# Kernel optimization log

Measured on AMD Instinct MI355X. Metric: run time of the kernel, lower is better.

The kernel has to match this reference:

```python
import jax, jax.numpy as jnp
import numpy as np

N = 2048
T = 4000
MAX_SPIKES = 512
V_RESET = 1.0
ALPHA = 0.01


def setup_inputs() -> dict:
    key = jax.random.key(0)
    k1, k2, k3, k4, k5 = jax.random.split(key, 5)
    ts = jnp.arange(T, dtype=jnp.float32) * (1.0 / T)  # [T] grid over [0, 1)
    v0 = 0.1 * jax.random.normal(k1, (N,), dtype=jnp.float32)
    i0 = 0.1 * jax.random.normal(k2, (N,), dtype=jnp.float32)
    ic = jax.random.uniform(k3, (N,), dtype=jnp.float32, minval=0.5, maxval=1.5)
    # _build_w: uniform weights in [0.5, 1), network mask all-False -> no zeroing
    w = jax.random.uniform(k4, (N, N), dtype=jnp.float32, minval=0.5, maxval=1.0)
    mu = jax.random.uniform(k5, (2,), dtype=jnp.float32, minval=0.5, maxval=1.0)
    return {"ts": ts, "v0": v0, "i0": i0, "ic": ic, "w": w, "mu": mu,
            "seed": 0, "max_spikes": MAX_SPIKES}


def reference(ts, v0, i0, ic, w, mu, seed, max_spikes):
    n = v0.shape[0]
    key = jax.random.key(seed)
    k_init, k_trans = jax.random.split(key)
    # s0 = log(U) - alpha  (negative; spike when s crosses 0)
    s0 = jnp.log(jax.random.uniform(k_init, (n,))) - ALPHA
    y0 = jnp.stack([v0, i0, s0], axis=-1)  # [n, 3]

    dts = ts[1:] - ts[:-1]
    steps = jnp.arange(ts.shape[0] - 1)
    tev0 = jnp.full((max_spikes,), jnp.inf, dtype=ts.dtype)
    yev0 = jnp.full((max_spikes, n, 3), jnp.inf, dtype=y0.dtype)
    et0 = jnp.zeros((max_spikes, n), dtype=bool)

    def drift(y):
        v, i, s = y[:, 0], y[:, 1], y[:, 2]
        dv = mu[0] * (i + ic - v)
        di = -mu[1] * i
        ds = jax.nn.softplus(v)  # intensity_fn
        return jnp.stack([dv, di, ds], axis=-1)

    def step(carry, inp):
        y, nsp, tev, yev, et = carry
        t_next, dt, idx = inp
        y1 = y + dt * drift(y)                 # Euler step
        ev = y1[:, 2] >= 0.0                   # cond_fn: y[n, 2] root crossing
        has = jnp.any(ev)
        eidx = jnp.argmax(ev)
        u = jax.random.uniform(jax.random.fold_in(k_trans, idx), (n,))
        # trans_fn: reset v, add weight row to all i, resample s for spikers
        v_t = y1[:, 0] - jnp.where(ev, V_RESET, 0.0)
        i_t = y1[:, 1] + w[eidx]
        s_t = jnp.where(ev, jnp.log(u) - ALPHA, y1[:, 2])
        y2 = jnp.where(has, jnp.stack([v_t, i_t, s_t], axis=-1), y1)
        rec = has & (nsp < max_spikes)
        widx = jnp.minimum(nsp, max_spikes - 1)
        tev = tev.at[widx].set(jnp.where(rec, t_next, tev[widx]))
        yev = yev.at[widx].set(jnp.where(rec, y1, yev[widx]))
        et = et.at[widx].set(jnp.where(rec, ev, et[widx]))
        nsp = nsp + has.astype(jnp.int32)
        return (y2, nsp, tev, yev, et), y2

    init = (y0, jnp.int32(0), tev0, yev0, et0)
    (_, num_spikes, tevents, yevents, event_types), ys_rest = jax.lax.scan(
        step, init, (ts[1:], dts, steps))
    ys = jnp.concatenate([y0[None], ys_rest], axis=0)  # [T, n, 3]
    return ys, tevents, yevents, event_types, num_spikes
```

## Files before the change

### kernel.cpp

```cpp
#include <hip/hip_runtime.h>
#include <stdint.h>

#define XLA_LOG_TAIL_A 1
#define XLA_USE_FMA    0

#if XLA_USE_FMA
#define MADD(a,b,c) __builtin_fmaf((a),(b),(c))
#else
#define MADD(a,b,c) ((a)*(b)+(c))
#endif

#define N_NEUR 2048
#define HALF_N 1024
#define CKPT   124

__device__ __forceinline__ uint32_t rotl32(uint32_t x, int r) {
  return (x << r) | (x >> (32 - r));
}

__device__ __forceinline__ void tf2x32(uint32_t k0, uint32_t k1,
                                       uint32_t& x0, uint32_t& x1) {
  const uint32_t k2 = k0 ^ k1 ^ 0x1BD11BDAu;
  x0 += k0; x1 += k1;
#define TF_R(r) { x0 += x1; x1 = rotl32(x1, r); x1 ^= x0; }
  TF_R(13) TF_R(15) TF_R(26) TF_R(6)
  x0 += k1; x1 += k2 + 1u;
  TF_R(17) TF_R(29) TF_R(16) TF_R(24)
  x0 += k2; x1 += k0 + 2u;
  TF_R(13) TF_R(15) TF_R(26) TF_R(6)
  x0 += k0; x1 += k1 + 3u;
  TF_R(17) TF_R(29) TF_R(16) TF_R(24)
  x0 += k1; x1 += k2 + 4u;
  TF_R(13) TF_R(15) TF_R(26) TF_R(6)
  x0 += k2; x1 += k0 + 5u;
#undef TF_R
}

__device__ __forceinline__ float u01_from_bits(uint32_t bits) {
#pragma clang fp contract(off)
  float f = __uint_as_float((bits >> 9) | 0x3f800000u);
  return f - 1.0f;
}

__device__ __forceinline__ float xla_log(float xin) {
#pragma clang fp contract(off)
  float t0 = fmaxf(xin, __uint_as_float(0x00800000u));
  uint32_t bits = __float_as_uint(t0);
  int em = (int)(bits >> 23) - 127;
  t0 = __uint_as_float((bits & 0x807fffffu) | 0x3f000000u);
  float e = 1.0f + (float)em;
  const bool mlt = t0 < (float)0.707106781186547524;
  float tmp1 = mlt ? t0 : 0.0f;
  t0 = t0 - 1.0f;
  e = e - (mlt ? 1.0f : 0.0f);
  t0 = t0 + tmp1;
  float x2 = t0 * t0;
  float x3 = x2 * t0;
  float y  = MADD(t0, (float)7.0376836292E-2, (float)-1.1514610310E-1);
  float ya = MADD(t0, (float)-1.2420140846E-1, (float)1.4249322787E-1);
  float yb = MADD(t0, (float)2.0000714765E-1, (float)-2.4999993993E-1);
  y  = MADD(y,  t0, (float)1.1676998740E-1);
  ya = MADD(ya, t0, (float)-1.6668057665E-1);
  yb = MADD(yb, t0, (float)3.3333331174E-1);
  y  = MADD(y, x3, ya);
  y  = MADD(y, x3, yb);
  y  = y * x3;
  float ey1 = e * (float)-2.12194440e-4;
  float hx2 = x2 * 0.5f;
  y = y + ey1;
  t0 = t0 - hx2;
  float ey2 = e * (float)0.693359375;
#if XLA_LOG_TAIL_A
  t0 = t0 + y;
  t0 = t0 + ey2;
#else
  t0 = t0 + ey2;
  t0 = t0 + y;
#endif
  if (xin == 0.0f) return -__builtin_inff();
  return t0;
}

__device__ __forceinline__ float xla_exp(float xin) {
#pragma clang fp contract(off)
  float x = fmaxf(xin, (float)-88.3762626647949);
  x = fminf(x, (float)88.3762626647950);
  float fx = floorf(MADD(x, (float)1.44269504088896341, 0.5f));
  float tmp = (float)0.693359375 * fx;
  float z = (float)-2.12194440e-4 * fx;
  x = x - tmp;
  x = x - z;
  z = x * x;
  float y = MADD(x, (float)1.9875691500E-4, (float)1.3981999507E-3);
  y = MADD(y, x, (float)8.3334519073E-3);
  y = MADD(y, x, (float)4.1665795894E-2);
  y = MADD(y, x, (float)1.6666665459E-1);
  y = MADD(y, x, (float)5.0000001201E-1);
  y = MADD(y, z, x);
  y = 1.0f + y;
  int n = (int)fx;
  float p2n = __uint_as_float((uint32_t)(n + 127) << 23);
  return fmaxf(y * p2n, xin);
}

__device__ __forceinline__ float xla_log1p(float x) {
#pragma clang fp contract(off)
  float fl = xla_log(x + 1.0f);
  float fs = ((-0.5f * x) + 1.0f) * x;
  return (fabsf(x) < (float)1e-4) ? fs : fl;
}

__device__ __forceinline__ float softplus_xla(float v) {
#pragma clang fp contract(off)
  if (v >= 16.0f) return v;
  float a = fabsf(v);
  float ex = xla_exp(-a);
  float lp = xla_log1p(ex);
  return fmaxf(v, 0.0f) + lp;
}

__global__ void snn_init(float* __restrict__ out, size_t inf_base,
                         size_t inf_cnt, size_t zero_cnt) {
  size_t i = (size_t)blockIdx.x * blockDim.x + threadIdx.x;
  size_t stride = (size_t)gridDim.x * blockDim.x;
  size_t total = inf_cnt + zero_cnt;
  for (size_t k = i; k < total; k += stride) {
    out[inf_base + k] = (k < inf_cnt) ? __builtin_inff() : 0.0f;
  }
}

__global__ __launch_bounds__(1024)
void snn_pre(const int* __restrict__ seedp, float* __restrict__ sres) {
#pragma clang fp contract(off)
  const int step = blockIdx.x;
  const int t = threadIdx.x;
  uint32_t seed = (uint32_t)seedp[0];
  uint32_t a0 = 0u, a1 = 2u; tf2x32(0u, seed, a0, a1);
  uint32_t b0 = 1u, b1 = 3u; tf2x32(0u, seed, b0, b1);
  uint32_t f0 = 0u, f1 = (uint32_t)step; tf2x32(a1, b1, f0, f1);
  uint32_t d0 = (uint32_t)t, d1 = (uint32_t)(t + HALF_N);
  tf2x32(f0, f1, d0, d1);
  float srA = xla_log(u01_from_bits(d0)) - 0.01f;
  float srB = xla_log(u01_from_bits(d1)) - 0.01f;
  sres[(size_t)step * N_NEUR + t] = srA;
  sres[(size_t)step * N_NEUR + HALF_N + t] = srB;
}

__global__ __launch_bounds__(512, 1)
void snn_evt(const float* __restrict__ ts, const float* __restrict__ v0,
             const float* __restrict__ i0, const float* __restrict__ ic,
             const float* __restrict__ w, const float* __restrict__ mu,
             const int* __restrict__ seedp, const float* __restrict__ sres,
             uint32_t* __restrict__ spk, float* __restrict__ out, int T, int MS) {
#pragma clang fp contract(off)
  const int tid = threadIdx.x;
  const int nb = tid * 4;
  const int wave = tid >> 6;
  const int lane = tid & 63;

  float* ys   = out;
  float* tev  = out + (size_t)T * N_NEUR * 3;
  float* etv  = tev + (size_t)MS + (size_t)MS * N_NEUR * 3;
  float* nspp = etv + (size_t)MS * N_NEUR;

  uint32_t seed = (uint32_t)seedp[0];
  uint32_t a0 = 0u, a1 = 2u; tf2x32(0u, seed, a0, a1);
  uint32_t b0 = 1u, b1 = 3u; tf2x32(0u, seed, b0, b1);
  const uint32_t ki0 = a0, ki1 = b0;

  const float m0 = mu[0], m1 = mu[1];

  float vvO[4];
  float ssE[4];
  bool  evO[4];
  float y1iP[4];
  float wEp[4], wOp[4];
  bool  hasEp = false, hasOp = false;
  float dtOp = 0.0f;
  float icv[4];
  float srE[4], srO[4];

  {
    float4 x = *(const float4*)&v0[nb];
    vvO[0]=x.x; vvO[1]=x.y; vvO[2]=x.z; vvO[3]=x.w;
  }
  {
    float4 x = *(const float4*)&i0[nb];
    y1iP[0]=x.x; y1iP[1]=x.y; y1iP[2]=x.z; y1iP[3]=x.w;
  }
  {
    float4 x = *(const float4*)&ic[nb];
    icv[0]=x.x; icv[1]=x.y; icv[2]=x.z; icv[3]=x.w;
  }
#pragma unroll
  for (int q = 0; q < 4; ++q) {
    int j = nb + q;
    uint32_t c0 = (uint32_t)(j < HALF_N ? j : j - HALF_N);
    uint32_t c1 = c0 + HALF_N;
    tf2x32(ki0, ki1, c0, c1);
    ssE[q] = xla_log(u01_from_bits(j < HALF_N ? c0 : c1)) - 0.01f;
    evO[q] = false;
    wEp[q] = 0.0f; wOp[q] = 0.0f;
  }
  {
    float4 x = *(const float4*)(sres + nb);
    srE[0]=x.x; srE[1]=x.y; srE[2]=x.z; srE[3]=x.w;
  }
  {
    float4 x = *(const float4*)(sres + N_NEUR + nb);
    srO[0]=x.x; srO[1]=x.y; srO[2]=x.z; srO[3]=x.w;
  }

  __shared__ alignas(16) uint32_t slot[2][16];
  __syncthreads();

  int nsp = 0;
  int next_ck = 0;
  float tsE = ts[0];
  const int pairs = (T - 1) >> 1;
  const int last_row = T - 2;

  for (int P = 0; P < pairs; ++P) {
    const int e = 2 * P;

    float vvE[4], iiE[4], y1iO_[4];
#pragma unroll
    for (int q = 0; q < 4; ++q) {
      float iiO = hasEp ? (y1iP[q] + wEp[q]) : y1iP[q];
      float dv  = m0 * ((iiO + icv[q]) - vvO[q]);
      float y1v = vvO[q] + dtOp * dv;
      float y1i = iiO + dtOp * ((-m1) * iiO);
      vvE[q] = y1v - (evO[q] ? 1.0f : 0.0f);
      y1iO_[q] = y1i;
    }
#pragma unroll
    for (int q = 0; q < 4; ++q)
      iiE[q] = hasOp ? (y1iO_[q] + wOp[q]) : y1iO_[q];

    if (e == next_ck) {
      float* yr = ys + ((size_t)e * N_NEUR + nb) * 3;
      ((float4*)yr)[0] = make_float4(vvE[0], iiE[0], ssE[0], vvE[1]);
      ((float4*)yr)[1] = make_float4(iiE[1], ssE[1], vvE[2], iiE[2]);
      ((float4*)yr)[2] = make_float4(ssE[2], vvE[3], iiE[3], ssE[3]);
      next_ck += CKPT;
    }

    const float tsE1 = ts[e + 1];
    const float tsE2 = ts[e + 2];
    const float dtE = tsE1 - tsE;
    const float dtO = tsE2 - tsE1;

    float y1iE[4], vvOn[4], ssEn[4];
    bool evE[4], evOn[4];
#pragma unroll
    for (int q = 0; q < 4; ++q) {
      float sp  = softplus_xla(vvE[q]);
      float y1s = ssE[q] + dtE * sp;
      evE[q] = (y1s >= 0.0f);
      float dv  = m0 * ((iiE[q] + icv[q]) - vvE[q]);
      float y1v = vvE[q] + dtE * dv;
      y1iE[q] = iiE[q] + dtE * ((-m1) * iiE[q]);
      vvOn[q] = y1v - (evE[q] ? 1.0f : 0.0f);
      float ssO_ = evE[q] ? srE[q] : y1s;
      float spO = softplus_xla(vvOn[q]);
      float y1sO = ssO_ + dtO * spO;
      evOn[q] = (y1sO >= 0.0f);
      ssEn[q] = evOn[q] ? srO[q] : y1sO;
    }

    {
      int lE = 4;
      if (evE[3]) lE = 3;
      if (evE[2]) lE = 2;
      if (evE[1]) lE = 1;
      if (evE[0]) lE = 0;
      int lO = 4;
      if (evOn[3]) lO = 3;
      if (evOn[2]) lO = 2;
      if (evOn[1]) lO = 1;
      if (evOn[0]) lO = 0;
      unsigned long long bE = __ballot(lE < 4);
      unsigned long long bO = __ballot(lO < 4);
      if (lane == 0) {
        uint32_t cE = 0xFFFFFFFFu, cO = 0xFFFFFFFFu;
        if (bE) cE = (uint32_t)__builtin_amdgcn_readlane(nb + lE, __builtin_ctzll(bE));
        if (bO) cO = (uint32_t)__builtin_amdgcn_readlane(nb + lO, __builtin_ctzll(bO));
        *(uint64_t*)&slot[P & 1][wave * 2] = ((uint64_t)cO << 32) | (uint64_t)cE;
      }
    }
    float srEn[4], srOn[4];
    {
      int re = e + 2;  if (re > last_row) re = last_row;
      int ro = e + 3;  if (ro > last_row) ro = last_row;
      float4 x = *(const float4*)(sres + (size_t)re * N_NEUR + nb);
      srEn[0]=x.x; srEn[1]=x.y; srEn[2]=x.z; srEn[3]=x.w;
      float4 y = *(const float4*)(sres + (size_t)ro * N_NEUR + nb);
      srOn[0]=y.x; srOn[1]=y.y; srOn[2]=y.z; srOn[3]=y.w;
    }

    __syncthreads();

    uint32_t gE, gO;
    {
      const uint4* rp = (const uint4*)&slot[P & 1][0];
      uint4 r0 = rp[0], r1 = rp[1], r2 = rp[2], r3 = rp[3];
      uint32_t a = r0.x < r1.x ? r0.x : r1.x;
      uint32_t b = r2.x < r3.x ? r2.x : r3.x;
      uint32_t c = r0.z < r1.z ? r0.z : r1.z;
      uint32_t d = r2.z < r3.z ? r2.z : r3.z;
      a = a < b ? a : b;  c = c < d ? c : d;
      gE = a < c ? a : c;
      uint32_t e1 = r0.y < r1.y ? r0.y : r1.y;
      uint32_t f1 = r2.y < r3.y ? r2.y : r3.y;
      uint32_t g1 = r0.w < r1.w ? r0.w : r1.w;
      uint32_t h1 = r2.w < r3.w ? r2.w : r3.w;
      e1 = e1 < f1 ? e1 : f1;  g1 = g1 < h1 ? g1 : h1;
      gO = e1 < g1 ? e1 : g1;
    }
    gE = (uint32_t)__builtin_amdgcn_readfirstlane((int)gE);
    gO = (uint32_t)__builtin_amdgcn_readfirstlane((int)gO);
    const bool hasE = (gE != 0xFFFFFFFFu);
    const bool hasO = (gO != 0xFFFFFFFFu);

    if (tid == 0) {
      spk[e] = ((uint32_t)nsp << 16) | (hasE ? (gE & 0xFFFFu) : 0xFFFFu);
      if (hasE && nsp < MS) tev[nsp] = tsE1;
    }
    int nspE = nsp + (hasE ? 1 : 0);
    if (tid == 0) {
      spk[e + 1] = ((uint32_t)nspE << 16) | (hasO ? (gO & 0xFFFFu) : 0xFFFFu);
      if (hasO && nspE < MS) tev[nspE] = tsE2;
    }
    nsp = nspE + (hasO ? 1 : 0);

    float wEn[4] = {0,0,0,0}, wOn[4] = {0,0,0,0};
    if (hasE) {
      float4 x = *(const float4*)&w[((size_t)gE << 11) + nb];
      wEn[0]=x.x; wEn[1]=x.y; wEn[2]=x.z; wEn[3]=x.w;
    }
    if (hasO) {
      float4 x = *(const float4*)&w[((size_t)gO << 11) + nb];
      wOn[0]=x.x; wOn[1]=x.y; wOn[2]=x.z; wOn[3]=x.w;
    }

#pragma unroll
    for (int q = 0; q < 4; ++q) {
      vvO[q] = vvOn[q];
      ssE[q] = ssEn[q];
      evO[q] = evOn[q];
      y1iP[q] = y1iE[q];
      wEp[q] = wEn[q];
      wOp[q] = wOn[q];
      srE[q] = srEn[q];
      srO[q] = srOn[q];
    }
    hasEp = hasE; hasOp = hasO;
    dtOp = dtO;
    tsE = tsE2;
  }

  if ((T - 1) & 1) {
    const int e = T - 2;
    float vvE[4], iiE[4];
#pragma unroll
    for (int q = 0; q < 4; ++q) {
      float iiO = hasEp ? (y1iP[q] + wEp[q]) : y1iP[q];
      float dv  = m0 * ((iiO + icv[q]) - vvO[q]);
      float y1v = vvO[q] + dtOp * dv;
      float y1i = iiO + dtOp * ((-m1) * iiO);
      vvE[q] = y1v - (evO[q] ? 1.0f : 0.0f);
      iiE[q] = hasOp ? (y1i + wOp[q]) : y1i;
    }
    if (e == next_ck) {
      float* yr = ys + ((size_t)e * N_NEUR + nb) * 3;
      ((float4*)yr)[0] = make_float4(vvE[0], iiE[0], ssE[0], vvE[1]);
      ((float4*)yr)[1] = make_float4(iiE[1], ssE[1], vvE[2], iiE[2]);
      ((float4*)yr)[2] = make_float4(ssE[2], vvE[3], iiE[3], ssE[3]);
    }
    const float tsE1 = ts[T - 1];
    const float dtE = tsE1 - tsE;
    bool evE[4];
#pragma unroll
    for (int q = 0; q < 4; ++q) {
      float sp  = softplus_xla(vvE[q]);
      float y1s = ssE[q] + dtE * sp;
      evE[q] = (y1s >= 0.0f);
    }
    int lE = 4;
    if (evE[3]) lE = 3;
    if (evE[2]) lE = 2;
    if (evE[1]) lE = 1;
    if (evE[0]) lE = 0;
    unsigned long long bE = __ballot(lE < 4);
    if (lane == 0) {
      uint32_t cE = 0xFFFFFFFFu;
      if (bE) cE = (uint32_t)__builtin_amdgcn_readlane(nb + lE, __builtin_ctzll(bE));
      *(uint64_t*)&slot[pairs & 1][wave * 2] =
          ((uint64_t)0xFFFFFFFFu << 32) | (uint64_t)cE;
    }
    __syncthreads();
    uint32_t gE;
    {
      const uint4* rp = (const uint4*)&slot[pairs & 1][0];
      uint4 r0 = rp[0], r1 = rp[1], r2 = rp[2], r3 = rp[3];
      uint32_t a = r0.x < r1.x ? r0.x : r1.x;
      uint32_t b = r2.x < r3.x ? r2.x : r3.x;
      uint32_t c = r0.z < r1.z ? r0.z : r1.z;
      uint32_t d = r2.z < r3.z ? r2.z : r3.z;
      a = a < b ? a : b;  c = c < d ? c : d;
      gE = a < c ? a : c;
    }
    gE = (uint32_t)__builtin_amdgcn_readfirstlane((int)gE);
    const bool hasE = (gE != 0xFFFFFFFFu);
    if (tid == 0) {
      spk[e] = ((uint32_t)nsp << 16) | (hasE ? (gE & 0xFFFFu) : 0xFFFFu);
      if (hasE && nsp < MS) tev[nsp] = tsE1;
    }
    nsp += hasE ? 1 : 0;
  }

  if (tid == 0) nspp[0] = (float)nsp;
}

__global__ __launch_bounds__(1024, 1)
void snn_rep(const float* __restrict__ ts, const float* __restrict__ ic,
             const float* __restrict__ w, const float* __restrict__ mu,
             const float* __restrict__ sres, const uint32_t* __restrict__ spk,
             float* __restrict__ out, int T, int MS) {
#pragma clang fp contract(off)
  const int seg = blockIdx.x >> 1;
  const int gn = (blockIdx.x & 1) * 1024 + threadIdx.x;
  const int lo = seg * CKPT;
  const int end = min(lo + CKPT, T - 1);

  float* ys  = out;
  float* tev = out + (size_t)T * N_NEUR * 3;
  float* yev = tev + (size_t)MS;
  float* etv = yev + (size_t)MS * N_NEUR * 3;

  const float* y0r = ys + ((size_t)lo * N_NEUR + gn) * 3;
  float vv = y0r[0];
  float ii = y0r[1];
  float ss = y0r[2];
  const float icv = ic[gn];
  const float m0 = mu[0], m1 = mu[1];
  float tp = ts[lo];

  for (int k = lo; k < end; ++k) {
    const float tn = ts[k + 1];
    const float dt = tn - tp;
    tp = tn;
    const uint32_t pk = spk[k];

    float sp  = softplus_xla(vv);
    float y1s = ss + dt * sp;
    const bool ev = (y1s >= 0.0f);
    float dv  = m0 * ((ii + icv) - vv);
    float y1v = vv + dt * dv;
    float y1i = ii + dt * ((-m1) * ii);

    const uint32_t e16 = pk & 0xFFFFu;
    const bool has = (e16 != 0xFFFFu);
    const uint32_t nsp = pk >> 16;

    float wv = 0.0f;
    if (has) wv = w[((size_t)e16 << 11) + gn];

    if (has && nsp < (uint32_t)MS) {
      float* ye = yev + ((size_t)nsp * N_NEUR + gn) * 3;
      ye[0] = y1v; ye[1] = y1i; ye[2] = y1s;
      etv[(size_t)nsp * N_NEUR + gn] = ev ? 1.0f : 0.0f;
    }

    ii = has ? (y1i + wv) : y1i;
    vv = y1v - (ev ? 1.0f : 0.0f);
    if (ev) ss = sres[(size_t)k * N_NEUR + gn]; else ss = y1s;

    float* yr = ys + ((size_t)(k + 1) * N_NEUR + gn) * 3;
    yr[0] = vv; yr[1] = ii; yr[2] = ss;
  }
}

template <bool USE_SRES>
__global__ __launch_bounds__(1024, 1)
void snn_sim(const float* __restrict__ ts, const float* __restrict__ v0,
             const float* __restrict__ i0, const float* __restrict__ ic,
             const float* __restrict__ w, const float* __restrict__ mu,
             const int* __restrict__ seedp, const float* __restrict__ sres,
             float* __restrict__ out, int T, int MS) {
#pragma clang fp contract(off)
  const int tid = threadIdx.x;
  const int nb = tid * 2;
  const int lane = tid & 63;

  float* ys   = out;
  float* tev  = out + (size_t)T * N_NEUR * 3;
  float* yev  = tev + (size_t)MS;
  float* etv  = yev + (size_t)MS * N_NEUR * 3;
  float* nspp = etv + (size_t)MS * N_NEUR;

  uint32_t seed = (uint32_t)seedp[0];
  uint32_t a0 = 0u, a1 = 2u; tf2x32(0u, seed, a0, a1);
  uint32_t b0 = 1u, b1 = 3u; tf2x32(0u, seed, b0, b1);
  const uint32_t ki0 = a0, ki1 = b0;
  const uint32_t kt0 = a1, kt1 = b1;

  float vv0, vv1, ii0, ii1, ss0, ss1, icv0, icv1;
  { float2 x = *(const float2*)&v0[nb]; vv0 = x.x; vv1 = x.y; }
  { float2 x = *(const float2*)&i0[nb]; ii0 = x.x; ii1 = x.y; }
  { float2 x = *(const float2*)&ic[nb]; icv0 = x.x; icv1 = x.y; }
  {
    uint32_t c0 = (uint32_t)(nb < HALF_N ? nb : nb - HALF_N);
    uint32_t c1 = c0 + HALF_N;
    tf2x32(ki0, ki1, c0, c1);
    ss0 = xla_log(u01_from_bits(nb < HALF_N ? c0 : c1)) - 0.01f;
  }
  {
    int j = nb + 1;
    uint32_t c0 = (uint32_t)(j < HALF_N ? j : j - HALF_N);
    uint32_t c1 = c0 + HALF_N;
    tf2x32(ki0, ki1, c0, c1);
    ss1 = xla_log(u01_from_bits(j < HALF_N ? c0 : c1)) - 0.01f;
  }
  const float m0 = mu[0], m1 = mu[1];

  {
    float* yr = ys + (size_t)nb * 3;
    ((float2*)yr)[0] = make_float2(vv0, ii0);
    ((float2*)yr)[1] = make_float2(ss0, vv1);
    ((float2*)yr)[2] = make_float2(ii1, ss1);
  }

  __shared__ uint32_t slot[4];
  if (tid < 4) slot[tid] = 0xFFFFFFFFu;
  __syncthreads();

  int nsp = 0;
  float tp = ts[0];
  const float* srp = USE_SRES ? (sres + nb) : nullptr;
  float* yrow = ys + (size_t)N_NEUR * 3 + (size_t)nb * 3;

  for (int k = 0; k < T - 1; ++k) {
    const float tn = ts[k + 1];
    const float dt = tn - tp;
    tp = tn;

    float sr0 = 0.0f, sr1 = 0.0f;
    if (USE_SRES) {
      float2 x = *(const float2*)srp;
      sr0 = x.x; sr1 = x.y;
      srp += N_NEUR;
    }

    float sp0 = softplus_xla(vv0);
    float sp1 = softplus_xla(vv1);
    float y1s0 = ss0 + dt * sp0;
    float y1s1 = ss1 + dt * sp1;
    const bool ev0 = (y1s0 >= 0.0f);
    const bool ev1 = (y1s1 >= 0.0f);

    int lidx = ev0 ? 0 : (ev1 ? 1 : 2);
    unsigned long long bm = __ballot(lidx < 2);
    if (lane == 0 && bm) {
      int fl = __builtin_ctzll(bm);
      uint32_t cand = (uint32_t)__builtin_amdgcn_readlane(nb + lidx, fl);
      atomicMin(&slot[k & 3], cand);
    }
    if (tid == 0) slot[(k + 1) & 3] = 0xFFFFFFFFu;

    float dv0 = m0 * ((ii0 + icv0) - vv0);
    float dv1 = m0 * ((ii1 + icv1) - vv1);
    float y1v0 = vv0 + dt * dv0;
    float y1v1 = vv1 + dt * dv1;
    float y1i0 = ii0 + dt * ((-m1) * ii0);
    float y1i1 = ii1 + dt * ((-m1) * ii1);

    __syncthreads();

    uint32_t gmin = (uint32_t)__builtin_amdgcn_readfirstlane((int)slot[k & 3]);
    const bool has = (gmin != 0xFFFFFFFFu);

    float wv0 = 0.0f, wv1 = 0.0f;
    if (has) {
      float2 x = *(const float2*)&w[((size_t)gmin << 11) + nb];
      wv0 = x.x; wv1 = x.y;
    }

    if (has && nsp < MS) {
      if (tid == 0) tev[nsp] = tn;
      float* ye = yev + ((size_t)nsp * N_NEUR + nb) * 3;
      ((float2*)ye)[0] = make_float2(y1v0, y1i0);
      ((float2*)ye)[1] = make_float2(y1s0, y1v1);
      ((float2*)ye)[2] = make_float2(y1i1, y1s1);
      *(float2*)(etv + (size_t)nsp * N_NEUR + nb) =
          make_float2(ev0 ? 1.0f : 0.0f, ev1 ? 1.0f : 0.0f);
    }
    nsp += has ? 1 : 0;

    ii0 = has ? (y1i0 + wv0) : y1i0;
    ii1 = has ? (y1i1 + wv1) : y1i1;
    vv0 = y1v0 - (ev0 ? 1.0f : 0.0f);
    vv1 = y1v1 - (ev1 ? 1.0f : 0.0f);
    if (USE_SRES) {
      ss0 = ev0 ? sr0 : y1s0;
      ss1 = ev1 ? sr1 : y1s1;
    } else {
      ss0 = y1s0; ss1 = y1s1;
      if (ev0 | ev1) {
        uint32_t f0 = 0u, f1 = (uint32_t)k;
        tf2x32(kt0, kt1, f0, f1);
        if (ev0) {
          uint32_t c0 = (uint32_t)(nb < HALF_N ? nb : nb - HALF_N);
          uint32_t c1 = c0 + HALF_N;
          tf2x32(f0, f1, c0, c1);
          ss0 = xla_log(u01_from_bits(nb < HALF_N ? c0 : c1)) - 0.01f;
        }
        if (ev1) {
          int j = nb + 1;
          uint32_t c0 = (uint32_t)(j < HALF_N ? j : j - HALF_N);
          uint32_t c1 = c0 + HALF_N;
          tf2x32(f0, f1, c0, c1);
          ss1 = xla_log(u01_from_bits(j < HALF_N ? c0 : c1)) - 0.01f;
        }
      }
    }

    ((float2*)yrow)[0] = make_float2(vv0, ii0);
    ((float2*)yrow)[1] = make_float2(ss0, vv1);
    ((float2*)yrow)[2] = make_float2(ii1, ss1);
    yrow += (size_t)N_NEUR * 3;
  }

  if (tid == 0) nspp[0] = (float)nsp;
}

extern "C" void kernel_launch(void* const* d_in, const int* in_sizes, int n_in,
                              void* d_out, int out_size, void* d_ws, size_t ws_size,
                              hipStream_t stream) {
  const float* ts = (const float*)d_in[0];
  const float* v0 = (const float*)d_in[1];
  const float* i0 = (const float*)d_in[2];
  const float* ic = (const float*)d_in[3];
  const float* w  = (const float*)d_in[4];
  const float* mu = (const float*)d_in[5];
  const int* seed = (const int*)d_in[6];

  const int T = in_sizes[0];
  const int N = in_sizes[1];
  long long rem = (long long)out_size - (long long)T * N * 3 - 1;
  int MS = (int)(rem / (1 + 4 * (long long)N));
  if (MS <= 0) MS = 512;

  size_t inf_base = (size_t)T * N * 3;
  size_t inf_cnt  = (size_t)MS + (size_t)MS * N * 3;
  size_t zero_cnt = (size_t)MS * N;
  snn_init<<<dim3(512), dim3(256), 0, stream>>>((float*)d_out, inf_base, inf_cnt, zero_cnt);

  size_t sres_bytes = (size_t)(T - 1) * (size_t)N * sizeof(float);
  size_t full_bytes = sres_bytes + (size_t)(T - 1) * sizeof(uint32_t);

  if (ws_size >= full_bytes) {
    float* sres = (float*)d_ws;
    uint32_t* spk = (uint32_t*)((char*)d_ws + sres_bytes);
    snn_pre<<<dim3(T - 1), dim3(1024), 0, stream>>>(seed, sres);
    snn_evt<<<dim3(1), dim3(512), 0, stream>>>(ts, v0, i0, ic, w, mu, seed,
                                               sres, spk, (float*)d_out, T, MS);
    int nseg = (T - 1 + CKPT - 1) / CKPT;
    snn_rep<<<dim3(nseg * 2), dim3(1024), 0, stream>>>(ts, ic, w, mu, sres, spk,
                                                       (float*)d_out, T, MS);
  } else if (ws_size >= sres_bytes) {
    snn_pre<<<dim3(T - 1), dim3(1024), 0, stream>>>(seed, (float*)d_ws);
    snn_sim<true><<<dim3(1), dim3(1024), 0, stream>>>(ts, v0, i0, ic, w, mu, seed,
                                                      (const float*)d_ws,
                                                      (float*)d_out, T, MS);
  } else {
    snn_sim<false><<<dim3(1), dim3(1024), 0, stream>>>(ts, v0, i0, ic, w, mu, seed,
                                                       nullptr, (float*)d_out, T, MS);
  }
}
```

Before: 3.097 ms.

## Widen event kernel to 1024 threads and reduce spike index via LDS atomicMin

The sequential event-detection kernel now runs 1024 threads with two neurons each instead of 512 threads with four, which halves per-thread serial work on the critical path. The per-wave slot array and 16-entry min-reduction after the barrier are replaced by LDS atomicMin into a four-deep ring of slots, each reset two pairs ahead. Loads of the next resample values and timestamps are moved earlier to overlap with compute. In exchange there are more waves per barrier (16 vs 8) and contended atomics on a single LDS word.

```diff
diff --git a/kernel.cpp b/kernel.cpp
--- a/kernel.cpp
+++ b/kernel.cpp
@@ -146,7 +146,7 @@
   sres[(size_t)step * N_NEUR + HALF_N + t] = srB;
 }
 
-__global__ __launch_bounds__(512, 1)
+__global__ __launch_bounds__(1024, 1)
 void snn_evt(const float* __restrict__ ts, const float* __restrict__ v0,
              const float* __restrict__ i0, const float* __restrict__ ic,
              const float* __restrict__ w, const float* __restrict__ mu,
@@ -154,8 +154,7 @@
              uint32_t* __restrict__ spk, float* __restrict__ out, int T, int MS) {
 #pragma clang fp contract(off)
   const int tid = threadIdx.x;
-  const int nb = tid * 4;
-  const int wave = tid >> 6;
+  const int nb = tid * 2;
   const int lane = tid & 63;
 
   float* ys   = out;
@@ -170,30 +169,16 @@
 
   const float m0 = mu[0], m1 = mu[1];
 
-  float vvO[4];
-  float ssE[4];
-  bool  evO[4];
-  float y1iP[4];
-  float wEp[4], wOp[4];
+  float vvO[2], ssE[2], y1iP[2], wEp[2], wOp[2], icv[2], srE[2], srO[2];
+  bool  evO[2];
   bool  hasEp = false, hasOp = false;
   float dtOp = 0.0f;
-  float icv[4];
-  float srE[4], srO[4];
-
-  {
-    float4 x = *(const float4*)&v0[nb];
-    vvO[0]=x.x; vvO[1]=x.y; vvO[2]=x.z; vvO[3]=x.w;
-  }
-  {
-    float4 x = *(const float4*)&i0[nb];
-    y1iP[0]=x.x; y1iP[1]=x.y; y1iP[2]=x.z; y1iP[3]=x.w;
-  }
-  {
-    float4 x = *(const float4*)&ic[nb];
-    icv[0]=x.x; icv[1]=x.y; icv[2]=x.z; icv[3]=x.w;
-  }
+
+  { float2 x = *(const float2*)&v0[nb]; vvO[0]=x.x; vvO[1]=x.y; }
+  { float2 x = *(const float2*)&i0[nb]; y1iP[0]=x.x; y1iP[1]=x.y; }
+  { float2 x = *(const float2*)&ic[nb]; icv[0]=x.x; icv[1]=x.y; }
 #pragma unroll
-  for (int q = 0; q < 4; ++q) {
+  for (int q = 0; q < 2; ++q) {
     int j = nb + q;
     uint32_t c0 = (uint32_t)(j < HALF_N ? j : j - HALF_N);
     uint32_t c1 = c0 + HALF_N;
@@ -202,16 +187,11 @@
     evO[q] = false;
     wEp[q] = 0.0f; wOp[q] = 0.0f;
   }
-  {
-    float4 x = *(const float4*)(sres + nb);
-    srE[0]=x.x; srE[1]=x.y; srE[2]=x.z; srE[3]=x.w;
-  }
-  {
-    float4 x = *(const float4*)(sres + N_NEUR + nb);
-    srO[0]=x.x; srO[1]=x.y; srO[2]=x.z; srO[3]=x.w;
-  }
-
-  __shared__ alignas(16) uint32_t slot[2][16];
+  { float2 x = *(const float2*)(sres + nb);          srE[0]=x.x; srE[1]=x.y; }
+  { float2 x = *(const float2*)(sres + N_NEUR + nb); srO[0]=x.x; srO[1]=x.y; }
+
+  __shared__ alignas(8) uint32_t slot[4][2];
+  if (tid < 8) ((uint32_t*)slot)[tid] = 0xFFFFFFFFu;
   __syncthreads();
 
   int nsp = 0;
@@ -223,9 +203,25 @@
   for (int P = 0; P < pairs; ++P) {
     const int e = 2 * P;
 
-    float vvE[4], iiE[4], y1iO_[4];
+    const float tsE1 = ts[e + 1];
+    const float tsE2 = ts[e + 2];
+    float srEn[2], srOn[2];
+    {
+      int re = e + 2;  if (re > last_row) re = last_row;
+      int ro = e + 3;  if (ro > last_row) ro = last_row;
+      float2 x = *(const float2*)(sres + (size_t)re * N_NEUR + nb);
+      srEn[0]=x.x; srEn[1]=x.y;
+      float2 y = *(const float2*)(sres + (size_t)ro * N_NEUR + nb);
+      srOn[0]=y.x; srOn[1]=y.y;
+    }
+    if (tid == 0) {
+      slot[(P + 2) & 3][0] = 0xFFFFFFFFu;
+      slot[(P + 2) & 3][1] = 0xFFFFFFFFu;
+    }
+
+    float vvE[2], iiE[2], y1iO_[2];
 #pragma unroll
-    for (int q = 0; q < 4; ++q) {
+    for (int q = 0; q < 2; ++q) {
       float iiO = hasEp ? (y1iP[q] + wEp[q]) : y1iP[q];
       float dv  = m0 * ((iiO + icv[q]) - vvO[q]);
       float y1v = vvO[q] + dtOp * dv;
@@ -234,26 +230,24 @@
       y1iO_[q] = y1i;
     }
 #pragma unroll
-    for (int q = 0; q < 4; ++q)
+    for (int q = 0; q < 2; ++q)
       iiE[q] = hasOp ? (y1iO_[q] + wOp[q]) : y1iO_[q];
 
     if (e == next_ck) {
       float* yr = ys + ((size_t)e * N_NEUR + nb) * 3;
-      ((float4*)yr)[0] = make_float4(vvE[0], iiE[0], ssE[0], vvE[1]);
-      ((float4*)yr)[1] = make_float4(iiE[1], ssE[1], vvE[2], iiE[2]);
-      ((float4*)yr)[2] = make_float4(ssE[2], vvE[3], iiE[3], ssE[3]);
+      ((float2*)yr)[0] = make_float2(vvE[0], iiE[0]);
+      ((float2*)yr)[1] = make_float2(ssE[0], vvE[1]);
+      ((float2*)yr)[2] = make_float2(iiE[1], ssE[1]);
       next_ck += CKPT;
     }
 
-    const float tsE1 = ts[e + 1];
-    const float tsE2 = ts[e + 2];
     const float dtE = tsE1 - tsE;
     const float dtO = tsE2 - tsE1;
 
-    float y1iE[4], vvOn[4], ssEn[4];
-    bool evE[4], evOn[4];
+    float y1iE[2], vvOn[2], ssEn[2];
+    bool evE[2], evOn[2];
 #pragma unroll
-    for (int q = 0; q < 4; ++q) {
+    for (int q = 0; q < 2; ++q) {
       float sp  = softplus_xla(vvE[q]);
       float y1s = ssE[q] + dtE * sp;
       evE[q] = (y1s >= 0.0f);
@@ -269,56 +263,27 @@
     }
 
     {
-      int lE = 4;
-      if (evE[3]) lE = 3;
-      if (evE[2]) lE = 2;
-      if (evE[1]) lE = 1;
-      if (evE[0]) lE = 0;
-      int lO = 4;
-      if (evOn[3]) lO = 3;
-      if (evOn[2]) lO = 2;
-      if (evOn[1]) lO = 1;
-      if (evOn[0]) lO = 0;
-      unsigned long long bE = __ballot(lE < 4);
-      unsigned long long bO = __ballot(lO < 4);
+      int lE = evE[0] ? 0 : (evE[1] ? 1 : 2);
+      int lO = evOn[0] ? 0 : (evOn[1] ? 1 : 2);
+      unsigned long long bE = __ballot(lE < 2);
+      unsigned long long bO = __ballot(lO < 2);
       if (lane == 0) {
-        uint32_t cE = 0xFFFFFFFFu, cO = 0xFFFFFFFFu;
-        if (bE) cE = (uint32_t)__builtin_amdgcn_readlane(nb + lE, __builtin_ctzll(bE));
-        if (bO) cO = (uint32_t)__builtin_amdgcn_readlane(nb + lO, __builtin_ctzll(bO));
-        *(uint64_t*)&slot[P & 1][wave * 2] = ((uint64_t)cO << 32) | (uint64_t)cE;
+        if (bE) {
+          uint32_t cE = (uint32_t)__builtin_amdgcn_readlane(nb + lE, __builtin_ctzll(bE));
+          atomicMin(&slot[P & 3][0], cE);
+        }
+        if (bO) {
+          uint32_t cO = (uint32_t)__builtin_amdgcn_readlane(nb + lO, __builtin_ctzll(bO));
+          atomicMin(&slot[P & 3][1], cO);
+        }
       }
     }
-    float srEn[4], srOn[4];
-    {
-      int re = e + 2;  if (re > last_row) re = last_row;
-      int ro = e + 3;  if (ro > last_row) ro = last_row;
-      float4 x = *(const float4*)(sres + (size_t)re * N_NEUR + nb);
-      srEn[0]=x.x; srEn[1]=x.y; srEn[2]=x.z; srEn[3]=x.w;
-      float4 y = *(const float4*)(sres + (size_t)ro * N_NEUR + nb);
-      srOn[0]=y.x; srOn[1]=y.y; srOn[2]=y.z; srOn[3]=y.w;
-    }
 
     __syncthreads();
 
-    uint32_t gE, gO;
-    {
-      const uint4* rp = (const uint4*)&slot[P & 1][0];
-      uint4 r0 = rp[0], r1 = rp[1], r2 = rp[2], r3 = rp[3];
-      uint32_t a = r0.x < r1.x ? r0.x : r1.x;
-      uint32_t b = r2.x < r3.x ? r2.x : r3.x;
-      uint32_t c = r0.z < r1.z ? r0.z : r1.z;
-      uint32_t d = r2.z < r3.z ? r2.z : r3.z;
-      a = a < b ? a : b;  c = c < d ? c : d;
-      gE = a < c ? a : c;
-      uint32_t e1 = r0.y < r1.y ? r0.y : r1.y;
-      uint32_t f1 = r2.y < r3.y ? r2.y : r3.y;
-      uint32_t g1 = r0.w < r1.w ? r0.w : r1.w;
-      uint32_t h1 = r2.w < r3.w ? r2.w : r3.w;
-      e1 = e1 < f1 ? e1 : f1;  g1 = g1 < h1 ? g1 : h1;
-      gO = e1 < g1 ? e1 : g1;
-    }
-    gE = (uint32_t)__builtin_amdgcn_readfirstlane((int)gE);
-    gO = (uint32_t)__builtin_amdgcn_readfirstlane((int)gO);
+    uint2 rr = *(const uint2*)&slot[P & 3][0];
+    uint32_t gE = (uint32_t)__builtin_amdgcn_readfirstlane((int)rr.x);
+    uint32_t gO = (uint32_t)__builtin_amdgcn_readfirstlane((int)rr.y);
     const bool hasE = (gE != 0xFFFFFFFFu);
     const bool hasO = (gO != 0xFFFFFFFFu);
 
@@ -333,18 +298,18 @@
     }
     nsp = nspE + (hasO ? 1 : 0);
 
-    float wEn[4] = {0,0,0,0}, wOn[4] = {0,0,0,0};
+    float wEn[2] = {0, 0}, wOn[2] = {0, 0};
     if (hasE) {
-      float4 x = *(const float4*)&w[((size_t)gE << 11) + nb];
-      wEn[0]=x.x; wEn[1]=x.y; wEn[2]=x.z; wEn[3]=x.w;
+      float2 x = *(const float2*)&w[((size_t)gE << 11) + nb];
+      wEn[0]=x.x; wEn[1]=x.y;
     }
     if (hasO) {
-      float4 x = *(const float4*)&w[((size_t)gO << 11) + nb];
-      wOn[0]=x.x; wOn[1]=x.y; wOn[2]=x.z; wOn[3]=x.w;
+      float2 x = *(const float2*)&w[((size_t)gO << 11) + nb];
+      wOn[0]=x.x; wOn[1]=x.y;
     }
 
 #pragma unroll
-    for (int q = 0; q < 4; ++q) {
+    for (int q = 0; q < 2; ++q) {
       vvO[q] = vvOn[q];
       ssE[q] = ssEn[q];
       evO[q] = evOn[q];
@@ -361,9 +326,9 @@
 
   if ((T - 1) & 1) {
     const int e = T - 2;
-    float vvE[4], iiE[4];
+    float vvE[2], iiE[2];
 #pragma unroll
-    for (int q = 0; q < 4; ++q) {
+    for (int q = 0; q < 2; ++q) {
       float iiO = hasEp ? (y1iP[q] + wEp[q]) : y1iP[q];
       float dv  = m0 * ((iiO + icv[q]) - vvO[q]);
       float y1v = vvO[q] + dtOp * dv;
@@ -373,44 +338,27 @@
     }
     if (e == next_ck) {
       float* yr = ys + ((size_t)e * N_NEUR + nb) * 3;
-      ((float4*)yr)[0] = make_float4(vvE[0], iiE[0], ssE[0], vvE[1]);
-      ((float4*)yr)[1] = make_float4(iiE[1], ssE[1], vvE[2], iiE[2]);
-      ((float4*)yr)[2] = make_float4(ssE[2], vvE[3], iiE[3], ssE[3]);
+      ((float2*)yr)[0] = make_float2(vvE[0], iiE[0]);
+      ((float2*)yr)[1] = make_float2(ssE[0], vvE[1]);
+      ((float2*)yr)[2] = make_float2(iiE[1], ssE[1]);
     }
     const float tsE1 = ts[T - 1];
     const float dtE = tsE1 - tsE;
-    bool evE[4];
+    bool evE[2];
 #pragma unroll
-    for (int q = 0; q < 4; ++q) {
+    for (int q = 0; q < 2; ++q) {
       float sp  = softplus_xla(vvE[q]);
       float y1s = ssE[q] + dtE * sp;
       evE[q] = (y1s >= 0.0f);
     }
-    int lE = 4;
-    if (evE[3]) lE = 3;
-    if (evE[2]) lE = 2;
-    if (evE[1]) lE = 1;
-    if (evE[0]) lE = 0;
-    unsigned long long bE = __ballot(lE < 4);
-    if (lane == 0) {
-      uint32_t cE = 0xFFFFFFFFu;
-      if (bE) cE = (uint32_t)__builtin_amdgcn_readlane(nb + lE, __builtin_ctzll(bE));
-      *(uint64_t*)&slot[pairs & 1][wave * 2] =
-          ((uint64_t)0xFFFFFFFFu << 32) | (uint64_t)cE;
+    int lE = evE[0] ? 0 : (evE[1] ? 1 : 2);
+    unsigned long long bE = __ballot(lE < 2);
+    if (lane == 0 && bE) {
+      uint32_t cE = (uint32_t)__builtin_amdgcn_readlane(nb + lE, __builtin_ctzll(bE));
+      atomicMin(&slot[pairs & 3][0], cE);
     }
     __syncthreads();
-    uint32_t gE;
-    {
-      const uint4* rp = (const uint4*)&slot[pairs & 1][0];
-      uint4 r0 = rp[0], r1 = rp[1], r2 = rp[2], r3 = rp[3];
-      uint32_t a = r0.x < r1.x ? r0.x : r1.x;
-      uint32_t b = r2.x < r3.x ? r2.x : r3.x;
-      uint32_t c = r0.z < r1.z ? r0.z : r1.z;
-      uint32_t d = r2.z < r3.z ? r2.z : r3.z;
-      a = a < b ? a : b;  c = c < d ? c : d;
-      gE = a < c ? a : c;
-    }
-    gE = (uint32_t)__builtin_amdgcn_readfirstlane((int)gE);
+    uint32_t gE = (uint32_t)__builtin_amdgcn_readfirstlane((int)slot[pairs & 3][0]);
     const bool hasE = (gE != 0xFFFFFFFFu);
     if (tid == 0) {
       spk[e] = ((uint32_t)nsp << 16) | (hasE ? (gE & 0xFFFFu) : 0xFFFFu);
@@ -663,8 +611,8 @@
     float* sres = (float*)d_ws;
     uint32_t* spk = (uint32_t*)((char*)d_ws + sres_bytes);
     snn_pre<<<dim3(T - 1), dim3(1024), 0, stream>>>(seed, sres);
-    snn_evt<<<dim3(1), dim3(512), 0, stream>>>(ts, v0, i0, ic, w, mu, seed,
-                                               sres, spk, (float*)d_out, T, MS);
+    snn_evt<<<dim3(1), dim3(1024), 0, stream>>>(ts, v0, i0, ic, w, mu, seed,
+                                                sres, spk, (float*)d_out, T, MS);
     int nseg = (T - 1 + CKPT - 1) / CKPT;
     snn_rep<<<dim3(nseg * 2), dim3(1024), 0, stream>>>(ts, ic, w, mu, sres, spk,
                                                        (float*)d_out, T, MS);
```

After: 2.978 ms. -3.8%, faster.
